# Performance work log

Hardware: AMD Instinct MI355X
Metric: run time of the kernel (lower is better)

The kernel has to match this reference:

```python
import jax, jax.numpy as jnp
import numpy as np

D_MODEL = 256
D_STATE = 1
HEADDIM = 32
NHEADS = D_MODEL // HEADDIM
HH = 64
WW = 64
BATCH = 2
L = HH * WW
D_IN_PROJ = (2 * D_MODEL + 2 * D_STATE + NHEADS) * 4


def _part1by1(n):
    n = n.astype(np.int64) & 0xFFFF
    n = (n | (n << 8)) & 0x00FF00FF
    n = (n | (n << 4)) & 0x0F0F0F0F
    n = (n | (n << 2)) & 0x33333333
    n = (n | (n << 1)) & 0x55555555
    return n


def _morton_indices(H, W):
    ys, xs = np.meshgrid(np.arange(H), np.arange(W), indexing='ij')
    ys, xs = ys.ravel(), xs.ravel()
    code_H = _part1by1(xs) | (_part1by1(ys) << 1)  # horizontal-first z-order
    code_V = _part1by1(ys) | (_part1by1(xs) << 1)  # vertical-first z-order
    mh = np.argsort(code_H, kind='stable').astype(np.int32)
    mv = np.argsort(code_V, kind='stable').astype(np.int32)
    ih = np.empty_like(mh); ih[mh] = np.arange(mh.size, dtype=np.int32)
    iv = np.empty_like(mv); iv[mv] = np.arange(mv.size, dtype=np.int32)
    return mh, mv, ih, iv


def setup_inputs() -> dict:
    key = jax.random.key(0)
    ks = jax.random.split(key, 12)
    x = jax.random.normal(ks[0], (BATCH, D_MODEL, HH, WW), dtype=jnp.float32)
    # RoPE tables: angles for L positions, HEADDIM/2 freqs
    freqs = 1.0 / (10000.0 ** (np.arange(0, HEADDIM, 2, dtype=np.float32) / HEADDIM))
    ang = np.outer(np.arange(L, dtype=np.float32), freqs)
    freqs_cos = jnp.asarray(np.cos(ang), dtype=jnp.float32)
    freqs_sin = jnp.asarray(np.sin(ang), dtype=jnp.float32)
    mh, mv, ih, iv = _morton_indices(HH, WW)
    # parameters
    W_in = jax.random.normal(ks[1], (D_MODEL, D_IN_PROJ), dtype=jnp.float32) * 0.02
    W_out = jax.random.normal(ks[2], (4 * D_MODEL, D_MODEL), dtype=jnp.float32) * 0.02
    conv_w = jax.random.normal(ks[3], (4, 2 * D_MODEL, 2 * D_MODEL, 3, 3), dtype=jnp.float32) * 0.02
    bn_gamma = jnp.ones((4, 2 * D_MODEL), dtype=jnp.float32)
    bn_beta = jnp.zeros((4, 2 * D_MODEL), dtype=jnp.float32)
    bn_mean = jax.random.normal(ks[4], (4, 2 * D_MODEL), dtype=jnp.float32) * 0.1
    bn_var = jax.random.uniform(ks[5], (4, 2 * D_MODEL), dtype=jnp.float32) * 0.5 + 0.5
    # dt bias init per module: inv softplus of dt ~ LogUniform(1e-3, 1e-1)
    u = np.asarray(jax.random.uniform(ks[6], (4, NHEADS)))
    dt = np.exp(u * (np.log(0.1) - np.log(0.001)) + np.log(0.001))
    dt_bias = jnp.asarray(dt + np.log(-np.expm1(-dt)), dtype=jnp.float32)
    A_log = jnp.log(jax.random.uniform(ks[7], (4, NHEADS), minval=1.0, maxval=16.0)).astype(jnp.float32)
    D = jnp.ones((4, NHEADS), dtype=jnp.float32)
    ln_gamma = jnp.ones((D_MODEL,), dtype=jnp.float32)
    ln_beta = jnp.zeros((D_MODEL,), dtype=jnp.float32)
    return dict(x=x, freqs_cos=freqs_cos, freqs_sin=freqs_sin,
                morton_H=jnp.asarray(mh), morton_V=jnp.asarray(mv),
                inv_H=jnp.asarray(ih), inv_V=jnp.asarray(iv),
                W_in=W_in, conv_w=conv_w, bn_gamma=bn_gamma, bn_beta=bn_beta,
                bn_mean=bn_mean, bn_var=bn_var, dt_bias=dt_bias, A_log=A_log,
                D=D, W_out=W_out, ln_gamma=ln_gamma, ln_beta=ln_beta)


def _rope(xh, cos, sin):
    # xh: [B,L,nh,hd]; complex multiply on (even,odd) pairs, matching view_as_complex
    xr, xi = xh[..., 0::2], xh[..., 1::2]
    c = cos[None, :, None, :]
    s = sin[None, :, None, :]
    out_r = xr * c - xi * s
    out_i = xr * s + xi * c
    return jnp.stack([out_r, out_i], axis=-1).reshape(xh.shape)


def _forward(x, freqs_cos, freqs_sin, morton_H, morton_V, inv_H, inv_V,
             W_in, conv_w, bn_gamma, bn_beta, bn_mean, bn_var,
             dt_bias, A_log, D, W_out, ln_gamma, ln_beta):
    B, C, H, W = x.shape
    Lh = H * W
    dim, ds, nh, hd = C, D_STATE, NHEADS, HEADDIM
    xf = x.reshape(B, C, Lh).transpose(0, 2, 1)            # [B,L,C]
    zxbcdt = xf @ W_in                                      # [B,L,d_in_proj]
    per = dim + (dim + 2 * ds) + nh
    specs = [(morton_H, inv_H, False), (morton_H, inv_H, True),
             (morton_V, inv_V, False), (morton_V, inv_V, True)]
    outs = []
    for d, (idx, iidx, flip) in enumerate(specs):
        blk = zxbcdt[..., d * per:(d + 1) * per]
        z = blk[..., :dim]
        xBC = blk[..., dim:2 * dim + 2 * ds]
        dt = blk[..., 2 * dim + 2 * ds:]
        xd, Bd, Cd = xBC[..., :dim], xBC[..., dim:dim + ds], xBC[..., dim + ds:]
        # depth-refine x,z with 3x3 conv + GELU + BN (eval)
        xz = jnp.concatenate([xd, z], axis=-1).transpose(0, 2, 1).reshape(B, 2 * C, H, W)
        xz = jax.lax.conv_general_dilated(xz, conv_w[d], (1, 1), 'SAME',
                                          dimension_numbers=('NCHW', 'OIHW', 'NCHW'))
        xz = jax.nn.gelu(xz)
        xz = (xz - bn_mean[d][None, :, None, None]) * jax.lax.rsqrt(bn_var[d] + 1e-3)[None, :, None, None] \
             * bn_gamma[d][None, :, None, None] + bn_beta[d][None, :, None, None]
        xz = xz.reshape(B, 2 * C, Lh).transpose(0, 2, 1)
        xd, zd = xz[..., :dim], xz[..., dim:]
        # morton reorder (+ flip for backward directions)
        def reord(a):
            a = jnp.take(a, idx, axis=1)
            return jnp.flip(a, axis=1) if flip else a
        xd, zd, Bd, Cd, dt = reord(xd), reord(zd), reord(Bd), reord(Cd), reord(dt)
        xh = _rope(xd.reshape(B, Lh, nh, hd), freqs_cos, freqs_sin)
        dtv = jax.nn.softplus(dt + dt_bias[d])              # [B,L,nh]
        A = -jnp.exp(A_log[d])                              # [nh]
        a = jnp.exp(dtv * A)                                # [B,L,nh]
        bterm = (dtv[..., None, None] * xh[..., None]) * Bd[:, :, None, None, :]  # [B,L,nh,hd,ds]
        def comb(c1, c2):
            a1, b1 = c1
            a2, b2 = c2
            return (a1 * a2, b1 * a2 + b2)
        _, h = jax.lax.associative_scan(comb, (a[..., None, None], bterm), axis=1)
        y = jnp.einsum('blhps,bls->blhp', h, Cd) + D[d][None, None, :, None] * xh
        y = y.reshape(B, Lh, dim) * (zd * jax.nn.sigmoid(zd))  # SiLU gate
        if flip:
            y = jnp.flip(y, axis=1)
        y = jnp.take(y, iidx, axis=1)                       # inverse morton
        outs.append(y)
    out = jnp.concatenate(outs, axis=-1) @ W_out            # [B,L,C]
    mu = out.mean(-1, keepdims=True)
    var = ((out - mu) ** 2).mean(-1, keepdims=True)
    out = (out - mu) * jax.lax.rsqrt(var + 1e-6) * ln_gamma + ln_beta
    return out.transpose(0, 2, 1).reshape(B, C, H, W)


def reference(x, freqs_cos, freqs_sin, morton_H, morton_V, inv_H, inv_V,
              W_in, conv_w, bn_gamma, bn_beta, bn_mean, bn_var,
              dt_bias, A_log, D, W_out, ln_gamma, ln_beta):
    return _forward(x, freqs_cos, freqs_sin, morton_H, morton_V, inv_H, inv_V,
                    W_in, conv_w, bn_gamma, bn_beta, bn_mean, bn_var,
                    dt_bias, A_log, D, W_out, ln_gamma, ln_beta)
```

## Files before the change

### kernel.cpp

```cpp
#include <hip/hip_runtime.h>
#include <math.h>

#define BATCH 2
#define CDIM 256
#define LLEN 4096
#define NH 8
#define HD 32
#define PER 522
#define NPROJ 2088
#define NPROJ_PAD 2112

typedef __attribute__((ext_vector_type(8))) short short8;
typedef __attribute__((ext_vector_type(4))) float f32x4;

static __device__ __forceinline__ ushort f2bf(float f) {
    unsigned u = __float_as_uint(f);
    u += 0x7fffu + ((u >> 16) & 1u);
    return (ushort)(u >> 16);
}
static __device__ __forceinline__ float bf2f(ushort u) {
    return __uint_as_float(((unsigned)u) << 16);
}

__global__ __launch_bounds__(256) void convert_wt(
    const float* __restrict__ W, ushort* __restrict__ Wt, int K, int N)
{
    __shared__ float tile[32][33];
    int n0 = blockIdx.x * 32, k0 = blockIdx.y * 32;
    int t = threadIdx.x;
    int nl = t & 31, kl = t >> 5;
    #pragma unroll
    for (int i = 0; i < 4; i++) {
        int n = n0 + nl;
        tile[kl + i * 8][nl] = (n < N) ? W[(long)(k0 + kl + i * 8) * N + n] : 0.f;
    }
    __syncthreads();
    int kl2 = t & 31, nl2 = t >> 5;
    #pragma unroll
    for (int i = 0; i < 4; i++)
        Wt[(long)(n0 + nl2 + i * 8) * K + k0 + kl2] = f2bf(tile[kl2][nl2 + i * 8]);
}

__global__ __launch_bounds__(256) void convert_x(
    const float* __restrict__ x, ushort* __restrict__ xbf)
{
    __shared__ float tile[32][33];
    int l0 = blockIdx.x * 32, c0 = blockIdx.y * 32, b = blockIdx.z;
    int t = threadIdx.x;
    int ll = t & 31, cl = t >> 5;
    #pragma unroll
    for (int i = 0; i < 4; i++)
        tile[cl + i * 8][ll] = x[((long)b * CDIM + c0 + cl + i * 8) * LLEN + l0 + ll];
    __syncthreads();
    int cl2 = t & 31, ll2 = t >> 5;
    #pragma unroll
    for (int i = 0; i < 4; i++)
        xbf[((long)b * LLEN + l0 + ll2 + i * 8) * CDIM + c0 + cl2] = f2bf(tile[cl2][ll2 + i * 8]);
}

__global__ __launch_bounds__(256) void convert_w(
    const float* __restrict__ cw, ushort* __restrict__ wbf)
{
    __shared__ ushort tmp[4608];
    int blk = blockIdx.x;
    int t = threadIdx.x;
    const float* src = cw + (long)blk * 4608;
    for (int q = t; q < 4608; q += 256) tmp[q] = f2bf(src[q]);
    __syncthreads();
    int d = blk >> 9, co = blk & 511;
    for (int q = t; q < 4608; q += 256) {
        int tt = q >> 9, ci = q & 511;
        wbf[(((long)(d * 9 + tt) * 512 + co) << 9) + ci] = tmp[ci * 9 + tt];
    }
}

__global__ __launch_bounds__(256) void gemm_in(
    const ushort* __restrict__ A, const ushort* __restrict__ Bt,
    ushort* __restrict__ cinb, float* __restrict__ bcdt)
{
    __shared__ ushort As[128][72];
    __shared__ ushort Bs[64][72];
    const int K = CDIM;
    int m0 = blockIdx.x * 128, n0 = blockIdx.y * 64;
    int t = threadIdx.x;
    int wave = t >> 6, lane = t & 63;
    int l15 = lane & 15, ko = lane >> 4;
    int mbase = wave * 32;

    f32x4 acc[2][4];
    #pragma unroll
    for (int mt = 0; mt < 2; mt++)
        #pragma unroll
        for (int nt = 0; nt < 4; nt++) acc[mt][nt] = (f32x4){0.f, 0.f, 0.f, 0.f};

    for (int k0 = 0; k0 < K; k0 += 64) {
        #pragma unroll
        for (int i = 0; i < 4; i++) {
            int g = t + 256 * i;
            int row = g >> 3, grp = g & 7;
            *(uint4*)&As[row][grp * 8] = *(const uint4*)&A[(long)(m0 + row) * K + k0 + grp * 8];
        }
        #pragma unroll
        for (int i = 0; i < 2; i++) {
            int g = t + 256 * i;
            int row = g >> 3, grp = g & 7;
            *(uint4*)&Bs[row][grp * 8] = *(const uint4*)&Bt[(long)(n0 + row) * K + k0 + grp * 8];
        }
        __syncthreads();
        #pragma unroll
        for (int kk = 0; kk < 2; kk++) {
            short8 a0 = *(const short8*)&As[mbase + l15][kk * 32 + ko * 8];
            short8 a1 = *(const short8*)&As[mbase + 16 + l15][kk * 32 + ko * 8];
            short8 bb[4];
            #pragma unroll
            for (int nt = 0; nt < 4; nt++)
                bb[nt] = *(const short8*)&Bs[nt * 16 + l15][kk * 32 + ko * 8];
            #pragma unroll
            for (int nt = 0; nt < 4; nt++) {
                acc[0][nt] = __builtin_amdgcn_mfma_f32_16x16x32_bf16(a0, bb[nt], acc[0][nt], 0, 0, 0);
                acc[1][nt] = __builtin_amdgcn_mfma_f32_16x16x32_bf16(a1, bb[nt], acc[1][nt], 0, 0, 0);
            }
        }
        __syncthreads();
    }
    #pragma unroll
    for (int nt = 0; nt < 4; nt++) {
        int n = n0 + nt * 16 + l15;
        if (n < NPROJ) {
            int d = n / PER;
            int r = n - d * PER;
            #pragma unroll
            for (int mt = 0; mt < 2; mt++)
                #pragma unroll
                for (int reg = 0; reg < 4; reg++) {
                    int m = m0 + mbase + mt * 16 + ko * 4 + reg;
                    int b = m >> 12, l = m & (LLEN - 1);
                    float v = acc[mt][nt][reg];
                    if (r < 512) {
                        int ch = (r < 256) ? (256 + r) : (r - 256);
                        cinb[(((long)d * BATCH + b) * LLEN + l) * 512 + ch] = f2bf(v);
                    } else {
                        bcdt[(long)m * 48 + d * 12 + (r - 512)] = v;
                    }
                }
        }
    }
}

__global__ __launch_bounds__(256) void gemm_bt(
    const ushort* __restrict__ A, const ushort* __restrict__ Bt, float* __restrict__ C,
    int K, int N)
{
    __shared__ ushort As[128][72];
    __shared__ ushort Bs[64][72];
    int m0 = blockIdx.x * 128, n0 = blockIdx.y * 64;
    int t = threadIdx.x;
    int wave = t >> 6, lane = t & 63;
    int l15 = lane & 15, ko = lane >> 4;
    int mbase = wave * 32;

    f32x4 acc[2][4];
    #pragma unroll
    for (int mt = 0; mt < 2; mt++)
        #pragma unroll
        for (int nt = 0; nt < 4; nt++) acc[mt][nt] = (f32x4){0.f, 0.f, 0.f, 0.f};

    for (int k0 = 0; k0 < K; k0 += 64) {
        #pragma unroll
        for (int i = 0; i < 4; i++) {
            int g = t + 256 * i;
            int row = g >> 3, grp = g & 7;
            *(uint4*)&As[row][grp * 8] = *(const uint4*)&A[(long)(m0 + row) * K + k0 + grp * 8];
        }
        #pragma unroll
        for (int i = 0; i < 2; i++) {
            int g = t + 256 * i;
            int row = g >> 3, grp = g & 7;
            *(uint4*)&Bs[row][grp * 8] = *(const uint4*)&Bt[(long)(n0 + row) * K + k0 + grp * 8];
        }
        __syncthreads();
        #pragma unroll
        for (int kk = 0; kk < 2; kk++) {
            short8 a0 = *(const short8*)&As[mbase + l15][kk * 32 + ko * 8];
            short8 a1 = *(const short8*)&As[mbase + 16 + l15][kk * 32 + ko * 8];
            short8 bb[4];
            #pragma unroll
            for (int nt = 0; nt < 4; nt++)
                bb[nt] = *(const short8*)&Bs[nt * 16 + l15][kk * 32 + ko * 8];
            #pragma unroll
            for (int nt = 0; nt < 4; nt++) {
                acc[0][nt] = __builtin_amdgcn_mfma_f32_16x16x32_bf16(a0, bb[nt], acc[0][nt], 0, 0, 0);
                acc[1][nt] = __builtin_amdgcn_mfma_f32_16x16x32_bf16(a1, bb[nt], acc[1][nt], 0, 0, 0);
            }
        }
        __syncthreads();
    }
    #pragma unroll
    for (int nt = 0; nt < 4; nt++) {
        int n = n0 + nt * 16 + l15;
        if (n < N) {
            #pragma unroll
            for (int mt = 0; mt < 2; mt++)
                #pragma unroll
                for (int reg = 0; reg < 4; reg++) {
                    int m = m0 + mbase + mt * 16 + ko * 4 + reg;
                    C[(long)m * N + n] = acc[mt][nt][reg];
                }
        }
    }
}

__global__ __launch_bounds__(256, 2) void conv_mfma(
    const ushort* __restrict__ cinb, const ushort* __restrict__ wbf,
    const float* __restrict__ bn_g, const float* __restrict__ bn_b,
    const float* __restrict__ bn_m, const float* __restrict__ bn_v,
    ushort* __restrict__ convb)
{
    __shared__ ushort in_s[6][4][66][8];

    int fid = blockIdx.x;
    int xcd = fid & 7;
    int k = fid >> 3;
    int slice = xcd * 4 + (k >> 5);
    int within = k & 31;
    int d = slice >> 3;
    int co0 = (slice & 7) * 64;
    int h0 = (within & 15) * 4;
    int b = within >> 4;
    int z = d * 2 + b;

    int t = threadIdx.x;
    int wave = t >> 6, lane = t & 63;
    int l15 = lane & 15, ko = lane >> 4;

    const ushort* conv_in = cinb + (long)z * LLEN * 512;
    ushort* conv_out = convb + (long)z * LLEN * 512;

    f32x4 acc[4][4];
    #pragma unroll
    for (int m = 0; m < 4; m++)
        #pragma unroll
        for (int nt = 0; nt < 4; nt++) acc[m][nt] = (f32x4){0.f, 0.f, 0.f, 0.f};

    const ushort* wtb = wbf + (long)d * 9 * 512 * 512 + (long)(co0 + l15) * 512 + ko * 8;

    for (int ci0 = 0; ci0 < 512; ci0 += 32) {
        for (int q = t; q < 1584; q += 256) {
            int oct = q & 3, pxg = q >> 2;
            int row = pxg / 66, px = pxg - row * 66;
            int hh = h0 + row - 1, wp = px - 1;
            uint4 val = make_uint4(0u, 0u, 0u, 0u);
            if (hh >= 0 && hh < 64 && wp >= 0 && wp < 64)
                val = *(const uint4*)&conv_in[(((long)hh) * 64 + wp) * 512 + ci0 + oct * 8];
            *(uint4*)&in_s[row][oct][px][0] = val;
        }
        const ushort* wp0 = wtb + ci0;
        short8 bw[4], bwn[4];
        #pragma unroll
        for (int nt = 0; nt < 4; nt++)
            bw[nt] = *(const short8*)&wp0[(long)nt * (16 * 512)];
        __syncthreads();
        #pragma unroll 1
        for (int tap = 0; tap < 9; tap++) {
            if (tap < 8) {
                const ushort* wq = wp0 + (long)(tap + 1) * (512 * 512);
                #pragma unroll
                for (int nt = 0; nt < 4; nt++)
                    bwn[nt] = *(const short8*)&wq[(long)nt * (16 * 512)];
            }
            int kh = (tap >= 6) ? 2 : ((tap >= 3) ? 1 : 0);
            int kw = tap - kh * 3;
            short8 av[4];
            #pragma unroll
            for (int m = 0; m < 4; m++)
                av[m] = *(const short8*)&in_s[wave + kh][ko][m * 16 + l15 + kw][0];
            #pragma unroll
            for (int m = 0; m < 4; m++)
                #pragma unroll
                for (int nt = 0; nt < 4; nt++)
                    acc[m][nt] = __builtin_amdgcn_mfma_f32_16x16x32_bf16(av[m], bw[nt], acc[m][nt], 0, 0, 0);
            #pragma unroll
            for (int nt = 0; nt < 4; nt++) bw[nt] = bwn[nt];
        }
        __syncthreads();
    }

    int hgl = h0 + wave;
    #pragma unroll
    for (int nt = 0; nt < 4; nt++) {
        int co = co0 + nt * 16 + l15;
        float mean = bn_m[d * 512 + co], var = bn_v[d * 512 + co];
        float g = bn_g[d * 512 + co], bbias = bn_b[d * 512 + co];
        float inv = rsqrtf(var + 1e-3f);
        #pragma unroll
        for (int m = 0; m < 4; m++)
            #pragma unroll
            for (int reg = 0; reg < 4; reg++) {
                int wc = m * 16 + ko * 4 + reg;
                float v = acc[m][nt][reg];
                float u = -1.5957691216057308f * (v + 0.044715f * v * v * v);
                v = v / (1.f + __expf(u));
                v = (v - mean) * inv * g + bbias;
                conv_out[((long)hgl * 64 + wc) * 512 + co] = f2bf(v);
            }
    }
}

__global__ __launch_bounds__(256) void scan_chunk(
    const float* __restrict__ bcdt, const ushort* __restrict__ conv_out,
    const int* __restrict__ mortonH, const int* __restrict__ mortonV,
    const float* __restrict__ fcos, const float* __restrict__ fsin,
    const float* __restrict__ dt_bias, const float* __restrict__ A_log,
    float* __restrict__ hfin, float* __restrict__ aprod_out)
{
    int chunk = blockIdx.x, b = blockIdx.y, d = blockIdx.z;
    const int* idx = (d < 2) ? mortonH : mortonV;
    int flip = d & 1;
    int c = threadIdx.x;
    int hh = c >> 5, p = c & 31;
    int i = p >> 1;
    float Acoef = -expf(A_log[d * 8 + hh]);
    float dtb = dt_bias[d * 8 + hh];
    float hstate = 0.f, aprod = 1.f;
    const ushort* cop = conv_out + (long)(d * BATCH + b) * LLEN * 512;
    for (int jj = 0; jj < 64; jj++) {
        int j = chunk * 64 + jj;
        int jsrc = flip ? (LLEN - 1 - j) : j;
        int src = idx[jsrc];
        const float* bc = bcdt + ((long)b * LLEN + src) * 48 + d * 12;
        float dtraw = bc[2 + hh] + dtb;
        float dtv = (dtraw > 20.f) ? dtraw : log1pf(expf(dtraw));
        float a = expf(dtv * Acoef);
        float Bd = bc[0];
        const ushort* xrow = cop + (long)src * 512;
        uint xz = *(const uint*)&xrow[hh * 32 + (p & ~1)];
        float xe = bf2f((ushort)(xz & 0xffff));
        float xo = bf2f((ushort)(xz >> 16));
        float cs = fcos[j * 16 + i], sn = fsin[j * 16 + i];
        float xh = (p & 1) ? (xe * sn + xo * cs) : (xe * cs - xo * sn);
        hstate = a * hstate + dtv * xh * Bd;
        aprod *= a;
    }
    long o = (((long)d * BATCH + b) * 64 + chunk) * 256 + c;
    hfin[o] = hstate;
    aprod_out[o] = aprod;
}

__global__ __launch_bounds__(256) void scan_chain(
    const float* __restrict__ hfin, const float* __restrict__ aprod, float* __restrict__ h0)
{
    int db = blockIdx.x;
    int c = threadIdx.x;
    float run = 0.f;
    for (int ch = 0; ch < 64; ch++) {
        long o = ((long)db * 64 + ch) * 256 + c;
        h0[o] = run;
        run = aprod[o] * run + hfin[o];
    }
}

__global__ __launch_bounds__(256) void scan_final(
    const float* __restrict__ bcdt, const ushort* __restrict__ conv_out,
    const int* __restrict__ mortonH, const int* __restrict__ mortonV,
    const float* __restrict__ fcos, const float* __restrict__ fsin,
    const float* __restrict__ dt_bias, const float* __restrict__ A_log, const float* __restrict__ Dp,
    const float* __restrict__ h0, ushort* __restrict__ ycat)
{
    int chunk = blockIdx.x, b = blockIdx.y, d = blockIdx.z;
    const int* idx = (d < 2) ? mortonH : mortonV;
    int flip = d & 1;
    int c = threadIdx.x;
    int hh = c >> 5, p = c & 31;
    int i = p >> 1;
    float Acoef = -expf(A_log[d * 8 + hh]);
    float dtb = dt_bias[d * 8 + hh];
    float Dv = Dp[d * 8 + hh];
    float hstate = h0[(((long)d * BATCH + b) * 64 + chunk) * 256 + c];
    const ushort* cop = conv_out + (long)(d * BATCH + b) * LLEN * 512;
    for (int jj = 0; jj < 64; jj++) {
        int j = chunk * 64 + jj;
        int jsrc = flip ? (LLEN - 1 - j) : j;
        int src = idx[jsrc];
        const float* bc = bcdt + ((long)b * LLEN + src) * 48 + d * 12;
        float dtraw = bc[2 + hh] + dtb;
        float dtv = (dtraw > 20.f) ? dtraw : log1pf(expf(dtraw));
        float a = expf(dtv * Acoef);
        float Bd = bc[0];
        float Cd = bc[1];
        const ushort* xrow = cop + (long)src * 512;
        uint xz = *(const uint*)&xrow[hh * 32 + (p & ~1)];
        float xe = bf2f((ushort)(xz & 0xffff));
        float xo = bf2f((ushort)(xz >> 16));
        float cs = fcos[j * 16 + i], sn = fsin[j * 16 + i];
        float xh = (p & 1) ? (xe * sn + xo * cs) : (xe * cs - xo * sn);
        hstate = a * hstate + dtv * xh * Bd;
        float y = hstate * Cd + Dv * xh;
        float zd = bf2f(xrow[256 + c]);
        y *= zd / (1.f + expf(-zd));
        ycat[((long)b * LLEN + src) * 1024 + d * 256 + c] = f2bf(y);
    }
}

__global__ __launch_bounds__(256) void ln_out(
    const float* __restrict__ pre, const float* __restrict__ g, const float* __restrict__ bta,
    float* __restrict__ out)
{
    int row = blockIdx.x;
    int c = threadIdx.x;
    float v = pre[(long)row * 256 + c];
    float s = v, s2 = v * v;
    #pragma unroll
    for (int o = 32; o > 0; o >>= 1) {
        s += __shfl_down(s, o);
        s2 += __shfl_down(s2, o);
    }
    __shared__ float ss[4], ss2[4];
    __shared__ float mean_s, inv_s;
    int wid = c >> 6;
    if ((c & 63) == 0) { ss[wid] = s; ss2[wid] = s2; }
    __syncthreads();
    if (c == 0) {
        float S = ss[0] + ss[1] + ss[2] + ss[3];
        float S2 = ss2[0] + ss2[1] + ss2[2] + ss2[3];
        float mean = S / 256.f;
        float var = S2 / 256.f - mean * mean;
        mean_s = mean;
        inv_s = rsqrtf(var + 1e-6f);
    }
    __syncthreads();
    float o = (v - mean_s) * inv_s * g[c] + bta[c];
    int b = row >> 12, l = row & (LLEN - 1);
    out[((long)b * 256 + c) * (long)LLEN + l] = o;
}

extern "C" void kernel_launch(void* const* d_in, const int* in_sizes, int n_in,
                              void* d_out, int out_size, void* d_ws, size_t ws_size,
                              hipStream_t stream)
{
    const float* x        = (const float*)d_in[0];
    const float* fcos     = (const float*)d_in[1];
    const float* fsin     = (const float*)d_in[2];
    const int*   mortonH  = (const int*)d_in[3];
    const int*   mortonV  = (const int*)d_in[4];
    const float* W_in     = (const float*)d_in[7];
    const float* conv_w   = (const float*)d_in[8];
    const float* bn_g     = (const float*)d_in[9];
    const float* bn_b     = (const float*)d_in[10];
    const float* bn_m     = (const float*)d_in[11];
    const float* bn_v     = (const float*)d_in[12];
    const float* dt_bias  = (const float*)d_in[13];
    const float* A_log    = (const float*)d_in[14];
    const float* Dp       = (const float*)d_in[15];
    const float* W_out    = (const float*)d_in[16];
    const float* ln_g     = (const float*)d_in[17];
    const float* ln_b     = (const float*)d_in[18];
    float* out = (float*)d_out;

    float* ws = (float*)d_ws;
    const long CONVB_OFF   = 0;
    const long HFIN_OFF    = CONVB_OFF + 8388608;
    const long APROD_OFF   = HFIN_OFF + 4L * BATCH * 64 * 256;
    const long H0_OFF      = APROD_OFF + 4L * BATCH * 64 * 256;
    const long BCDT_OFF    = H0_OFF + 4L * BATCH * 64 * 256;
    const long WBF_OFF     = BCDT_OFF + (long)BATCH * LLEN * 48;
    const long CINB_OFF    = WBF_OFF + 4718592;
    const long XBF_OFF     = CINB_OFF + 8388608;
    const long WINT_OFF    = XBF_OFF + 1048576;
    const long WOUTT_OFF   = WINT_OFF + 270336;
    const long YCATB_OFF   = WOUTT_OFF + 131072;
    const long PRE_OFF     = YCATB_OFF + 4194304;

    ushort* convb   = (ushort*)(ws + CONVB_OFF);
    float* hfin     = ws + HFIN_OFF;
    float* aprod    = ws + APROD_OFF;
    float* h0       = ws + H0_OFF;
    float* bcdt     = ws + BCDT_OFF;
    ushort* wbf     = (ushort*)(ws + WBF_OFF);
    ushort* cinb    = (ushort*)(ws + CINB_OFF);
    ushort* xbf     = (ushort*)(ws + XBF_OFF);
    ushort* wint    = (ushort*)(ws + WINT_OFF);
    ushort* woutt   = (ushort*)(ws + WOUTT_OFF);
    ushort* ycatb   = (ushort*)(ws + YCATB_OFF);
    float* pre      = ws + PRE_OFF;

    convert_w<<<4 * 512, 256, 0, stream>>>(conv_w, wbf);
    convert_wt<<<dim3(NPROJ_PAD / 32, CDIM / 32), 256, 0, stream>>>(W_in, wint, CDIM, NPROJ);
    convert_wt<<<dim3(CDIM / 32, 1024 / 32), 256, 0, stream>>>(W_out, woutt, 1024, CDIM);
    convert_x<<<dim3(LLEN / 32, CDIM / 32, BATCH), 256, 0, stream>>>(x, xbf);

    gemm_in<<<dim3(64, NPROJ_PAD / 64), 256, 0, stream>>>(xbf, wint, cinb, bcdt);

    conv_mfma<<<1024, 256, 0, stream>>>(
        cinb, wbf, bn_g, bn_b, bn_m, bn_v, convb);

    scan_chunk<<<dim3(64, BATCH, 4), 256, 0, stream>>>(
        bcdt, convb, mortonH, mortonV, fcos, fsin, dt_bias, A_log, hfin, aprod);
    scan_chain<<<4 * BATCH, 256, 0, stream>>>(hfin, aprod, h0);
    scan_final<<<dim3(64, BATCH, 4), 256, 0, stream>>>(
        bcdt, convb, mortonH, mortonV, fcos, fsin, dt_bias, A_log, Dp, h0, ycatb);

    gemm_bt<<<dim3(64, CDIM / 64), 256, 0, stream>>>(ycatb, woutt, pre, 1024, CDIM);

    ln_out<<<BATCH * LLEN, 256, 0, stream>>>(pre, ln_g, ln_b, out);
}
```

Measured before the change: 493.3 us.

## Streamline conv tile staging, unroll weight prefetch, fold scan chain into final scan

The conv kernel zeroes the LDS halo once, before the channel loop, then stages each input slice with a fixed per-thread mapping. This removes the per-element divide and bounds checks from the inner copy. The weight prefetch is restructured into three rotating register buffers so each tap's MFMAs overlap with the next tap's loads, including across channel slices. The separate scan_chain launch is removed: each scan_final block recomputes its starting state serially from the per-chunk summaries, which saves a launch and a global round trip but adds up to 64 serial steps per block.

```diff
diff --git a/kernel.cpp b/kernel.cpp
--- a/kernel.cpp
+++ b/kernel.cpp
@@ -9,6 +9,7 @@
 #define PER 522
 #define NPROJ 2088
 #define NPROJ_PAD 2112
+#define TAPSZ (512 * 512)
 
 typedef __attribute__((ext_vector_type(8))) short short8;
 typedef __attribute__((ext_vector_type(4))) float f32x4;
@@ -235,6 +236,26 @@
 
     const ushort* conv_in = cinb + (long)z * LLEN * 512;
     ushort* conv_out = convb + (long)z * LLEN * 512;
+    ushort* lds = &in_s[0][0][0][0];
+
+    uint4 z4 = make_uint4(0u, 0u, 0u, 0u);
+    if (t < 48) {
+        int row = t >> 3, oc = (t >> 1) & 3, side = t & 1;
+        *(uint4*)&lds[(((row * 4 + oc) * 66) + side * 65) * 8] = z4;
+    }
+    if (h0 == 0) {
+        int u = t;
+        *(uint4*)&lds[u * 8] = z4;
+        if (t < 8) *(uint4*)&lds[(256 + t) * 8] = z4;
+    }
+    if (h0 == 60) {
+        *(uint4*)&lds[(1320 + t) * 8] = z4;
+        if (t < 8) *(uint4*)&lds[(1320 + 256 + t) * 8] = z4;
+    }
+
+    int soct = t >> 6, spx = t & 63;
+    const ushort* gbase = conv_in + (long)(h0 - 1) * 32768 + spx * 512 + soct * 8;
+    int lbase = ((soct * 66) + spx + 1) * 8;
 
     f32x4 acc[4][4];
     #pragma unroll
@@ -242,45 +263,47 @@
         #pragma unroll
         for (int nt = 0; nt < 4; nt++) acc[m][nt] = (f32x4){0.f, 0.f, 0.f, 0.f};
 
-    const ushort* wtb = wbf + (long)d * 9 * 512 * 512 + (long)(co0 + l15) * 512 + ko * 8;
-
-    for (int ci0 = 0; ci0 < 512; ci0 += 32) {
-        for (int q = t; q < 1584; q += 256) {
-            int oct = q & 3, pxg = q >> 2;
-            int row = pxg / 66, px = pxg - row * 66;
-            int hh = h0 + row - 1, wp = px - 1;
-            uint4 val = make_uint4(0u, 0u, 0u, 0u);
-            if (hh >= 0 && hh < 64 && wp >= 0 && wp < 64)
-                val = *(const uint4*)&conv_in[(((long)hh) * 64 + wp) * 512 + ci0 + oct * 8];
-            *(uint4*)&in_s[row][oct][px][0] = val;
-        }
-        const ushort* wp0 = wtb + ci0;
-        short8 bw[4], bwn[4];
+    const ushort* wtb = wbf + (long)d * 9 * TAPSZ + (long)(co0 + l15) * 512 + ko * 8;
+
+    auto loadw = [&](short8* dst, const ushort* src) {
         #pragma unroll
         for (int nt = 0; nt < 4; nt++)
-            bw[nt] = *(const short8*)&wp0[(long)nt * (16 * 512)];
+            dst[nt] = *(const short8*)&src[(long)nt * (16 * 512)];
+    };
+    auto mfma_tap = [&](int kh, int kw, short8* bw) {
+        short8 av[4];
+        #pragma unroll
+        for (int m = 0; m < 4; m++)
+            av[m] = *(const short8*)&in_s[wave + kh][ko][m * 16 + l15 + kw][0];
+        #pragma unroll
+        for (int m = 0; m < 4; m++)
+            #pragma unroll
+            for (int nt = 0; nt < 4; nt++)
+                acc[m][nt] = __builtin_amdgcn_mfma_f32_16x16x32_bf16(av[m], bw[nt], acc[m][nt], 0, 0, 0);
+    };
+
+    short8 bwA[4], bwB[4], bwC[4];
+    loadw(bwA, wtb);
+
+    for (int s = 0; s < 16; ++s) {
+        const ushort* gs = gbase + s * 32;
+        #pragma unroll
+        for (int i = 0; i < 6; i++) {
+            if ((unsigned)(h0 + i - 1) < 64u)
+                *(uint4*)&lds[lbase + i * 2112] = *(const uint4*)(gs + (long)i * 32768);
+        }
         __syncthreads();
+        const ushort* ws0 = wtb + s * 32;
         #pragma unroll 1
-        for (int tap = 0; tap < 9; tap++) {
-            if (tap < 8) {
-                const ushort* wq = wp0 + (long)(tap + 1) * (512 * 512);
-                #pragma unroll
-                for (int nt = 0; nt < 4; nt++)
-                    bwn[nt] = *(const short8*)&wq[(long)nt * (16 * 512)];
-            }
-            int kh = (tap >= 6) ? 2 : ((tap >= 3) ? 1 : 0);
-            int kw = tap - kh * 3;
-            short8 av[4];
-            #pragma unroll
-            for (int m = 0; m < 4; m++)
-                av[m] = *(const short8*)&in_s[wave + kh][ko][m * 16 + l15 + kw][0];
-            #pragma unroll
-            for (int m = 0; m < 4; m++)
-                #pragma unroll
-                for (int nt = 0; nt < 4; nt++)
-                    acc[m][nt] = __builtin_amdgcn_mfma_f32_16x16x32_bf16(av[m], bw[nt], acc[m][nt], 0, 0, 0);
-            #pragma unroll
-            for (int nt = 0; nt < 4; nt++) bw[nt] = bwn[nt];
+        for (int tp = 0; tp < 3; tp++) {
+            const ushort* wt = ws0 + (long)(3 * tp) * TAPSZ;
+            loadw(bwB, wt + TAPSZ);
+            mfma_tap(tp, 0, bwA);
+            loadw(bwC, wt + 2 * TAPSZ);
+            mfma_tap(tp, 1, bwB);
+            if (tp < 2)      loadw(bwA, wt + 3 * TAPSZ);
+            else if (s < 15) loadw(bwA, wtb + (s + 1) * 32);
+            mfma_tap(tp, 2, bwC);
         }
         __syncthreads();
     }
@@ -346,25 +369,12 @@
     aprod_out[o] = aprod;
 }
 
-__global__ __launch_bounds__(256) void scan_chain(
-    const float* __restrict__ hfin, const float* __restrict__ aprod, float* __restrict__ h0)
-{
-    int db = blockIdx.x;
-    int c = threadIdx.x;
-    float run = 0.f;
-    for (int ch = 0; ch < 64; ch++) {
-        long o = ((long)db * 64 + ch) * 256 + c;
-        h0[o] = run;
-        run = aprod[o] * run + hfin[o];
-    }
-}
-
 __global__ __launch_bounds__(256) void scan_final(
     const float* __restrict__ bcdt, const ushort* __restrict__ conv_out,
     const int* __restrict__ mortonH, const int* __restrict__ mortonV,
     const float* __restrict__ fcos, const float* __restrict__ fsin,
     const float* __restrict__ dt_bias, const float* __restrict__ A_log, const float* __restrict__ Dp,
-    const float* __restrict__ h0, ushort* __restrict__ ycat)
+    const float* __restrict__ hfin, const float* __restrict__ aprod, ushort* __restrict__ ycat)
 {
     int chunk = blockIdx.x, b = blockIdx.y, d = blockIdx.z;
     const int* idx = (d < 2) ? mortonH : mortonV;
@@ -375,7 +385,14 @@
     float Acoef = -expf(A_log[d * 8 + hh]);
     float dtb = dt_bias[d * 8 + hh];
     float Dv = Dp[d * 8 + hh];
-    float hstate = h0[(((long)d * BATCH + b) * 64 + chunk) * 256 + c];
+    float hstate = 0.f;
+    {
+        long ob = ((long)d * BATCH + b) * 64;
+        for (int ch = 0; ch < chunk; ch++) {
+            long o = (ob + ch) * 256 + c;
+            hstate = aprod[o] * hstate + hfin[o];
+        }
+    }
     const ushort* cop = conv_out + (long)(d * BATCH + b) * LLEN * 512;
     for (int jj = 0; jj < 64; jj++) {
         int j = chunk * 64 + jj;
@@ -473,7 +490,6 @@
     ushort* convb   = (ushort*)(ws + CONVB_OFF);
     float* hfin     = ws + HFIN_OFF;
     float* aprod    = ws + APROD_OFF;
-    float* h0       = ws + H0_OFF;
     float* bcdt     = ws + BCDT_OFF;
     ushort* wbf     = (ushort*)(ws + WBF_OFF);
     ushort* cinb    = (ushort*)(ws + CINB_OFF);
@@ -495,9 +511,8 @@
 
     scan_chunk<<<dim3(64, BATCH, 4), 256, 0, stream>>>(
         bcdt, convb, mortonH, mortonV, fcos, fsin, dt_bias, A_log, hfin, aprod);
-    scan_chain<<<4 * BATCH, 256, 0, stream>>>(hfin, aprod, h0);
     scan_final<<<dim3(64, BATCH, 4), 256, 0, stream>>>(
-        bcdt, convb, mortonH, mortonV, fcos, fsin, dt_bias, A_log, Dp, h0, ycatb);
+        bcdt, convb, mortonH, mortonV, fcos, fsin, dt_bias, A_log, Dp, hfin, aprod, ycatb);
 
     gemm_bt<<<dim3(64, CDIM / 64), 256, 0, stream>>>(ycatb, woutt, pre, 1024, CDIM);
 
```

Result: slower. 540.1 us (+9.5%).

## Fold chunk-carry chain into scan_final and use fast exp/log intrinsics

Applied to the files above, without the earlier changes.

Removes the separate scan_chain kernel. Each scan_final block now recomputes its own starting state by walking the carries (aprod, hfin) of all earlier chunks, which drops one launch and one serial 8-block kernel. The cost is redundant work: up to 63 extra dependent load-multiply steps per thread in later chunks. The change also swaps expf and log1pf for the __expf and __logf intrinsics in the scan kernels, cutting transcendental cost at slightly lower accuracy.

```diff
diff --git a/kernel.cpp b/kernel.cpp
--- a/kernel.cpp
+++ b/kernel.cpp
@@ -319,7 +319,7 @@
     int c = threadIdx.x;
     int hh = c >> 5, p = c & 31;
     int i = p >> 1;
-    float Acoef = -expf(A_log[d * 8 + hh]);
+    float Acoef = -__expf(A_log[d * 8 + hh]);
     float dtb = dt_bias[d * 8 + hh];
     float hstate = 0.f, aprod = 1.f;
     const ushort* cop = conv_out + (long)(d * BATCH + b) * LLEN * 512;
@@ -329,8 +329,8 @@
         int src = idx[jsrc];
         const float* bc = bcdt + ((long)b * LLEN + src) * 48 + d * 12;
         float dtraw = bc[2 + hh] + dtb;
-        float dtv = (dtraw > 20.f) ? dtraw : log1pf(expf(dtraw));
-        float a = expf(dtv * Acoef);
+        float dtv = (dtraw > 20.f) ? dtraw : __logf(1.f + __expf(dtraw));
+        float a = __expf(dtv * Acoef);
         float Bd = bc[0];
         const ushort* xrow = cop + (long)src * 512;
         uint xz = *(const uint*)&xrow[hh * 32 + (p & ~1)];
@@ -346,25 +346,12 @@
     aprod_out[o] = aprod;
 }
 
-__global__ __launch_bounds__(256) void scan_chain(
-    const float* __restrict__ hfin, const float* __restrict__ aprod, float* __restrict__ h0)
-{
-    int db = blockIdx.x;
-    int c = threadIdx.x;
-    float run = 0.f;
-    for (int ch = 0; ch < 64; ch++) {
-        long o = ((long)db * 64 + ch) * 256 + c;
-        h0[o] = run;
-        run = aprod[o] * run + hfin[o];
-    }
-}
-
 __global__ __launch_bounds__(256) void scan_final(
     const float* __restrict__ bcdt, const ushort* __restrict__ conv_out,
     const int* __restrict__ mortonH, const int* __restrict__ mortonV,
     const float* __restrict__ fcos, const float* __restrict__ fsin,
     const float* __restrict__ dt_bias, const float* __restrict__ A_log, const float* __restrict__ Dp,
-    const float* __restrict__ h0, ushort* __restrict__ ycat)
+    const float* __restrict__ hfin, const float* __restrict__ aprod, ushort* __restrict__ ycat)
 {
     int chunk = blockIdx.x, b = blockIdx.y, d = blockIdx.z;
     const int* idx = (d < 2) ? mortonH : mortonV;
@@ -372,10 +359,17 @@
     int c = threadIdx.x;
     int hh = c >> 5, p = c & 31;
     int i = p >> 1;
-    float Acoef = -expf(A_log[d * 8 + hh]);
+    float Acoef = -__expf(A_log[d * 8 + hh]);
     float dtb = dt_bias[d * 8 + hh];
     float Dv = Dp[d * 8 + hh];
-    float hstate = h0[(((long)d * BATCH + b) * 64 + chunk) * 256 + c];
+    float hstate = 0.f;
+    {
+        long ob = ((long)d * BATCH + b) * 64;
+        for (int ch = 0; ch < chunk; ch++) {
+            long o = (ob + ch) * 256 + c;
+            hstate = aprod[o] * hstate + hfin[o];
+        }
+    }
     const ushort* cop = conv_out + (long)(d * BATCH + b) * LLEN * 512;
     for (int jj = 0; jj < 64; jj++) {
         int j = chunk * 64 + jj;
@@ -383,8 +377,8 @@
         int src = idx[jsrc];
         const float* bc = bcdt + ((long)b * LLEN + src) * 48 + d * 12;
         float dtraw = bc[2 + hh] + dtb;
-        float dtv = (dtraw > 20.f) ? dtraw : log1pf(expf(dtraw));
-        float a = expf(dtv * Acoef);
+        float dtv = (dtraw > 20.f) ? dtraw : __logf(1.f + __expf(dtraw));
+        float a = __expf(dtv * Acoef);
         float Bd = bc[0];
         float Cd = bc[1];
         const ushort* xrow = cop + (long)src * 512;
@@ -396,7 +390,7 @@
         hstate = a * hstate + dtv * xh * Bd;
         float y = hstate * Cd + Dv * xh;
         float zd = bf2f(xrow[256 + c]);
-        y *= zd / (1.f + expf(-zd));
+        y *= zd / (1.f + __expf(-zd));
         ycat[((long)b * LLEN + src) * 1024 + d * 256 + c] = f2bf(y);
     }
 }
@@ -473,7 +467,6 @@
     ushort* convb   = (ushort*)(ws + CONVB_OFF);
     float* hfin     = ws + HFIN_OFF;
     float* aprod    = ws + APROD_OFF;
-    float* h0       = ws + H0_OFF;
     float* bcdt     = ws + BCDT_OFF;
     ushort* wbf     = (ushort*)(ws + WBF_OFF);
     ushort* cinb    = (ushort*)(ws + CINB_OFF);
@@ -495,9 +488,8 @@
 
     scan_chunk<<<dim3(64, BATCH, 4), 256, 0, stream>>>(
         bcdt, convb, mortonH, mortonV, fcos, fsin, dt_bias, A_log, hfin, aprod);
-    scan_chain<<<4 * BATCH, 256, 0, stream>>>(hfin, aprod, h0);
     scan_final<<<dim3(64, BATCH, 4), 256, 0, stream>>>(
-        bcdt, convb, mortonH, mortonV, fcos, fsin, dt_bias, A_log, Dp, h0, ycatb);
+        bcdt, convb, mortonH, mortonV, fcos, fsin, dt_bias, A_log, Dp, hfin, aprod, ycatb);
 
     gemm_bt<<<dim3(64, CDIM / 64), 256, 0, stream>>>(ycatb, woutt, pre, 1024, CDIM);
 
```

Result: faster. 426.4 us (-13.6%).
